# Kernel optimization log

Measured on AMD Instinct MI355X. Metric: run time of the kernel, lower is better.

## Reference

```python
import jax, jax.numpy as jnp
import numpy as np

B, S, D, H, FF = 4, 2048, 512, 8, 2048
W = 128  # local attention window size (hardcoded in module)
DH = D // H


def _ln(x, g, b, eps=1e-5):
    m = x.mean(-1, keepdims=True)
    v = ((x - m) ** 2).mean(-1, keepdims=True)
    return (x - m) / jnp.sqrt(v + eps) * g + b


def setup_inputs() -> dict:
    key = jax.random.key(0)
    ks = jax.random.split(key, 10)
    s = 0.02
    return {
        "src": jax.random.normal(ks[0], (B, S, D), jnp.float32),
        # global nn.MultiheadAttention params
        "in_proj_w": jax.random.normal(ks[1], (3 * D, D), jnp.float32) * s,
        "in_proj_b": jnp.zeros((3 * D,), jnp.float32),
        "out_proj_w": jax.random.normal(ks[2], (D, D), jnp.float32) * s,
        "out_proj_b": jnp.zeros((D,), jnp.float32),
        # LocalMHA params (prenorm LN, fused qkv no-bias, out proj no-bias)
        "ln_g": jnp.ones((D,), jnp.float32),
        "ln_b": jnp.zeros((D,), jnp.float32),
        "qkv_w": jax.random.normal(ks[3], (3 * D, D), jnp.float32) * s,
        "to_out_w": jax.random.normal(ks[4], (D, D), jnp.float32) * s,
        # glFusion + FFN + norms
        "gl_w": jax.random.normal(ks[5], (D, 2 * D), jnp.float32) * s,
        "gl_b": jnp.zeros((D,), jnp.float32),
        "norm1_g": jnp.ones((D,), jnp.float32),
        "norm1_b": jnp.zeros((D,), jnp.float32),
        "lin1_w": jax.random.normal(ks[6], (FF, D), jnp.float32) * s,
        "lin1_b": jnp.zeros((FF,), jnp.float32),
        "lin2_w": jax.random.normal(ks[7], (D, FF), jnp.float32) * s,
        "lin2_b": jnp.zeros((D,), jnp.float32),
        "norm2_g": jnp.ones((D,), jnp.float32),
        "norm2_b": jnp.zeros((D,), jnp.float32),
    }


def _forward(src, in_proj_w, in_proj_b, out_proj_w, out_proj_b, ln_g, ln_b,
             qkv_w, to_out_w, gl_w, gl_b, norm1_g, norm1_b,
             lin1_w, lin1_b, lin2_w, lin2_b, norm2_g, norm2_b):
    b, s, d = src.shape
    scale = DH ** -0.5

    def heads(x):  # (b, s, d) -> (b, H, s, DH)
        return x.reshape(b, s, H, DH).transpose(0, 2, 1, 3)

    # ---- global full MHA (no mask) ----
    qkv = src @ in_proj_w.T + in_proj_b
    qg, kg, vg = (heads(t) for t in jnp.split(qkv, 3, axis=-1))
    att = jax.nn.softmax(jnp.einsum('bhid,bhjd->bhij', qg, kg) * scale, axis=-1)
    go = jnp.einsum('bhij,bhjd->bhid', att, vg).transpose(0, 2, 1, 3).reshape(b, s, d)
    go = go @ out_proj_w.T + out_proj_b

    # ---- local windowed causal MHA with rotary (window=128, look_backward=1) ----
    x = _ln(src, ln_g, ln_b)  # prenorm
    ql, kl, vl = (heads(t) for t in jnp.split(x @ qkv_w.T, 3, axis=-1))

    pos = jnp.arange(s)
    inv_freq = 1.0 / (10000.0 ** (jnp.arange(0, DH, 2, dtype=jnp.float32) / DH))
    freqs = pos[:, None].astype(jnp.float32) * inv_freq[None, :]
    emb = jnp.concatenate([freqs, freqs], axis=-1)  # (s, DH)
    cos, sin = jnp.cos(emb), jnp.sin(emb)

    def rope(t):
        h = DH // 2
        t1, t2 = t[..., :h], t[..., h:]
        return t * cos + jnp.concatenate([-t2, t1], axis=-1) * sin

    ql, kl = rope(ql), rope(kl)
    ql = ql * scale

    nw = s // W
    qw = ql.reshape(b, H, nw, W, DH)
    kw = kl.reshape(b, H, nw, W, DH)
    vw = vl.reshape(b, H, nw, W, DH)

    def look_back(t):  # concat previous window with current: (b,H,nw,2W,DH)
        prev = jnp.pad(t, ((0, 0), (0, 0), (1, 0), (0, 0), (0, 0)))[:, :, :-1]
        return jnp.concatenate([prev, t], axis=3)

    bk, bv = look_back(kw), look_back(vw)

    qpos = pos.reshape(nw, W)
    kpos = jnp.concatenate(
        [jnp.concatenate([jnp.full((1, W), -1, pos.dtype), qpos[:-1]], axis=0), qpos],
        axis=1)  # (nw, 2W)
    mask = (kpos[:, None, :] >= 0) & (kpos[:, None, :] <= qpos[:, :, None])  # (nw,W,2W)

    sc = jnp.einsum('bhnid,bhnjd->bhnij', qw, bk)
    sc = jnp.where(mask, sc, jnp.finfo(sc.dtype).min)
    at = jax.nn.softmax(sc, axis=-1)
    lo = jnp.einsum('bhnij,bhnjd->bhnid', at, bv).reshape(b, H, s, DH)
    lo = lo.transpose(0, 2, 1, 3).reshape(b, s, d) @ to_out_w.T

    # ---- fuse global+local, residual, norms, FFN ----
    src2 = jnp.concatenate([go, lo], axis=-1) @ gl_w.T + gl_b
    h1 = _ln(src + src2, norm1_g, norm1_b)
    ff = jax.nn.relu(h1 @ lin1_w.T + lin1_b) @ lin2_w.T + lin2_b
    return _ln(h1 + ff, norm2_g, norm2_b)


def reference(src, in_proj_w, in_proj_b, out_proj_w, out_proj_b, ln_g, ln_b,
              qkv_w, to_out_w, gl_w, gl_b, norm1_g, norm1_b,
              lin1_w, lin1_b, lin2_w, lin2_b, norm2_g, norm2_b):
    return _forward(src, in_proj_w, in_proj_b, out_proj_w, out_proj_b, ln_g, ln_b,
                    qkv_w, to_out_w, gl_w, gl_b, norm1_g, norm1_b,
                    lin1_w, lin1_b, lin2_w, lin2_b, norm2_g, norm2_b)
```

## Files before the change

### kernel.cpp

```cpp
#include <hip/hip_runtime.h>
#include <math.h>

#define B_  4
#define S_  2048
#define D_  512
#define H_  8
#define FF_ 2048
#define W_  128
#define DH_ 64
#define NW_ 16
#define TRD (3*D_)
#define MR_ (B_*S_)

typedef __attribute__((ext_vector_type(8))) short short8;
typedef __attribute__((ext_vector_type(4))) float f32x4;

__device__ __forceinline__ short f2bf(float f) {
    unsigned u = __float_as_uint(f);
    unsigned r = (u + 0x7fff + ((u >> 16) & 1)) >> 16;
    return (short)r;
}
__device__ __forceinline__ float bf2f(ushort u) {
    return __uint_as_float(((unsigned)u) << 16);
}
__device__ __forceinline__ void gload_lds16(const ushort* g, short* l) {
    __builtin_amdgcn_global_load_lds(
        (const __attribute__((address_space(1))) void*)g,
        (__attribute__((address_space(3))) void*)l, 16, 0, 0);
}

struct CvtJobs { const float* s[8]; ushort* d[8]; int n[8]; };

__global__ __launch_bounds__(256) void cvt_kernel(CvtJobs jobs)
{
    int i4 = (blockIdx.x * 256 + threadIdx.x) * 4;
    #pragma unroll
    for (int j = 0; j < 8; j++) {
        if (i4 < jobs.n[j]) {
            float4 v = *(const float4*)(jobs.s[j] + i4);
            ushort4 o;
            o.x = (ushort)f2bf(v.x); o.y = (ushort)f2bf(v.y);
            o.z = (ushort)f2bf(v.z); o.w = (ushort)f2bf(v.w);
            *(ushort4*)(jobs.d[j] + i4) = o;
        }
    }
}

__global__ __launch_bounds__(256) void gemm_bf16_kernel(
    const ushort* __restrict__ A, int lda,
    const ushort* __restrict__ Wt,
    const float* __restrict__ bias,
    ushort* __restrict__ C, int ldc,
    int K, int relu)
{
    __shared__ short As[128 * 64];
    __shared__ short Bs[128 * 64];
    const int tid  = threadIdx.x;
    const int w    = tid >> 6;
    const int lane = tid & 63;
    const int quad = lane >> 4;
    const int x    = lane & 15;
    const int wr = w >> 1, wc = w & 1;
    const int bm = blockIdx.y * 128;
    const int bn = blockIdx.x * 128;

    const int srow = w * 32 + (lane >> 3);
    const int scol = ((lane & 7) ^ (lane >> 3)) * 8;

    f32x4 acc[4][4];
    #pragma unroll
    for (int i = 0; i < 4; i++)
        #pragma unroll
        for (int j = 0; j < 4; j++) acc[i][j] = (f32x4)0.f;

    for (int k0 = 0; k0 < K; k0 += 64) {
        __syncthreads();
        #pragma unroll
        for (int c = 0; c < 4; c++) {
            const ushort* ga = A + (size_t)(bm + srow + c * 8) * lda + k0 + scol;
            gload_lds16(ga, &As[(w * 32 + c * 8) * 64]);
            const ushort* gb = Wt + (size_t)(bn + srow + c * 8) * K + k0 + scol;
            gload_lds16(gb, &Bs[(w * 32 + c * 8) * 64]);
        }
        __syncthreads();

        #pragma unroll
        for (int kc = 0; kc < 2; kc++) {
            short8 af[4], bf[4];
            #pragma unroll
            for (int i = 0; i < 4; i++) {
                int row = wr * 64 + i * 16 + x;
                int pcg = (kc * 4 + quad) ^ (x & 7);
                af[i] = *(const short8*)&As[row * 64 + pcg * 8];
            }
            #pragma unroll
            for (int j = 0; j < 4; j++) {
                int row = wc * 64 + j * 16 + x;
                int pcg = (kc * 4 + quad) ^ (x & 7);
                bf[j] = *(const short8*)&Bs[row * 64 + pcg * 8];
            }
            #pragma unroll
            for (int i = 0; i < 4; i++)
                #pragma unroll
                for (int j = 0; j < 4; j++)
                    acc[i][j] = __builtin_amdgcn_mfma_f32_16x16x32_bf16(af[i], bf[j], acc[i][j], 0, 0, 0);
        }
    }

    #pragma unroll
    for (int i = 0; i < 4; i++) {
        #pragma unroll
        for (int r = 0; r < 4; r++) {
            size_t row = (size_t)(bm + wr * 64 + i * 16 + quad * 4 + r);
            #pragma unroll
            for (int j = 0; j < 4; j++) {
                int col = bn + wc * 64 + j * 16 + x;
                float v = acc[i][j][r] + (bias ? bias[col] : 0.f);
                if (relu) v = v > 0.f ? v : 0.f;
                C[row * ldc + col] = (ushort)f2bf(v);
            }
        }
    }
}

__device__ __forceinline__ float wave_sum64(float v) {
    #pragma unroll
    for (int off = 32; off > 0; off >>= 1) v += __shfl_xor(v, off, 64);
    return v;
}
__device__ __forceinline__ void load8(const float* p, float* v) {
    *(float4*)&v[0] = *(const float4*)p;
    *(float4*)&v[4] = *(const float4*)(p + 4);
}
__device__ __forceinline__ void load8(const ushort* p, float* v) {
    short8 s = *(const short8*)p;
    #pragma unroll
    for (int i = 0; i < 8; i++) v[i] = bf2f((ushort)s[i]);
}
__device__ __forceinline__ void store8(float* p, const float* v) {
    *(float4*)p       = make_float4(v[0], v[1], v[2], v[3]);
    *(float4*)(p + 4) = make_float4(v[4], v[5], v[6], v[7]);
}
__device__ __forceinline__ void store8(ushort* p, const float* v) {
    short8 s;
    #pragma unroll
    for (int i = 0; i < 8; i++) s[i] = f2bf(v[i]);
    *(short8*)p = s;
}

template <typename TA, typename TB, typename TO>
__global__ __launch_bounds__(256) void addln_kernel(
    const TA* __restrict__ a, const TB* __restrict__ b,
    const float* __restrict__ g, const float* __restrict__ be,
    TO* __restrict__ out)
{
    const int lane = threadIdx.x & 63;
    const int row  = blockIdx.x * 4 + (threadIdx.x >> 6);
    const size_t base = (size_t)row * D_ + lane * 8;
    float v[8];
    load8(a + base, v);
    if (b) {
        float wv[8];
        load8(b + base, wv);
        #pragma unroll
        for (int i = 0; i < 8; i++) v[i] += wv[i];
    }
    float s = 0.f;
    #pragma unroll
    for (int i = 0; i < 8; i++) s += v[i];
    float mean = wave_sum64(s) * (1.0f / 512.0f);
    float vs = 0.f;
    #pragma unroll
    for (int i = 0; i < 8; i++) { float d = v[i] - mean; vs += d * d; }
    float var = wave_sum64(vs) * (1.0f / 512.0f);
    float r = rsqrtf(var + 1e-5f);
    const int c = lane * 8;
    float t[8];
    #pragma unroll
    for (int i = 0; i < 8; i++) t[i] = (v[i] - mean) * r * g[c + i] + be[c + i];
    store8(out + base, t);
}

__global__ __launch_bounds__(256) void transpose_v_kernel(
    const ushort* __restrict__ qkv, ushort* __restrict__ vt)
{
    __shared__ ushort T[64][72];
    const int t  = threadIdx.x;
    const int s0 = blockIdx.x * 64;
    const int bh = blockIdx.y;
    const int b = bh >> 3, h = bh & 7;
    {
        int row = t >> 2, col = (t & 3) * 16;
        const ushort* src = qkv + ((size_t)(b * S_) + s0 + row) * TRD + 2 * D_ + h * DH_ + col;
        *(short8*)&T[row][col]     = *(const short8*)src;
        *(short8*)&T[row][col + 8] = *(const short8*)(src + 8);
    }
    __syncthreads();
    {
        int d = t >> 2, sc = (t & 3) * 16;
        ushort tmp[16];
        #pragma unroll
        for (int k = 0; k < 16; k++) tmp[k] = T[sc + k][d];
        ushort* dst = vt + ((size_t)bh * DH_ + d) * S_ + s0 + sc;
        *(short8*)dst       = *(const short8*)&tmp[0];
        *(short8*)(dst + 8) = *(const short8*)&tmp[8];
    }
}

#define PP 136

__global__ __launch_bounds__(256) void attn_global_mfma_kernel(
    const ushort* __restrict__ qkv, const ushort* __restrict__ vt,
    ushort* __restrict__ out)
{
    __shared__ short Ks[128 * 64];
    __shared__ short Vt[64 * 128];
    __shared__ short Pb[4 * 16 * PP];

    const int tid  = threadIdx.x;
    const int w    = tid >> 6;
    const int lane = tid & 63;
    const int quad = lane >> 4;
    const int x    = lane & 15;
    const int bh = blockIdx.y;
    const int b = bh >> 3, h = bh & 7;
    const int qbase = blockIdx.x * 64;
    const size_t bS = (size_t)b * S_;
    const size_t vbase = (size_t)bh * DH_;

    short8 aq[2];
    {
        const ushort* qp = qkv + (bS + qbase + w * 16 + x) * TRD + h * DH_;
        #pragma unroll
        for (int kc = 0; kc < 2; kc++) {
            short8 raw = *(const short8*)(qp + kc * 32 + quad * 8);
            #pragma unroll
            for (int j = 0; j < 8; j++)
                aq[kc][j] = f2bf(bf2f((ushort)raw[j]) * 0.125f);
        }
    }

    f32x4 o[4];
    #pragma unroll
    for (int dt = 0; dt < 4; dt++) o[dt] = (f32x4)0.f;
    float m[4], l[4];
    #pragma unroll
    for (int r = 0; r < 4; r++) { m[r] = -3.0e38f; l[r] = 0.f; }

    short* Pw = &Pb[w * 16 * PP];

    for (int kt = 0; kt < S_; kt += 128) {
        __syncthreads();
        #pragma unroll
        for (int c = 0; c < 4; c++) {
            int key = w * 32 + c * 8 + (lane >> 3);
            int cg  = (lane & 7) ^ (lane >> 3);
            const ushort* gk = qkv + (bS + kt + key) * TRD + D_ + h * DH_ + cg * 8;
            gload_lds16(gk, &Ks[(w * 32 + c * 8) * 64]);
        }
        #pragma unroll
        for (int c = 0; c < 4; c++) {
            int row = w * 16 + c * 4 + (lane >> 4);
            int cg  = (lane & 15) ^ (row & 7);
            const ushort* gv = vt + (vbase + row) * S_ + kt + cg * 8;
            gload_lds16(gv, &Vt[(w * 16 + c * 4) * 128]);
        }
        __syncthreads();

        f32x4 sc[8];
        #pragma unroll
        for (int nt = 0; nt < 8; nt++) {
            sc[nt] = (f32x4)0.f;
            #pragma unroll
            for (int kc = 0; kc < 2; kc++) {
                int pcg = (kc * 4 + quad) ^ (x & 7);
                short8 bk = *(const short8*)&Ks[(nt * 16 + x) * 64 + pcg * 8];
                sc[nt] = __builtin_amdgcn_mfma_f32_16x16x32_bf16(aq[kc], bk, sc[nt], 0, 0, 0);
            }
        }

        #pragma unroll
        for (int r = 0; r < 4; r++) {
            float mx = sc[0][r];
            #pragma unroll
            for (int nt = 1; nt < 8; nt++) mx = fmaxf(mx, sc[nt][r]);
            #pragma unroll
            for (int off = 1; off < 16; off <<= 1) mx = fmaxf(mx, __shfl_xor(mx, off, 64));
            float mnew = fmaxf(m[r], mx);
            float alpha = __expf(m[r] - mnew);
            m[r] = mnew;
            float psum = 0.f;
            #pragma unroll
            for (int nt = 0; nt < 8; nt++) {
                float p = __expf(sc[nt][r] - mnew);
                sc[nt][r] = p;
                psum += p;
            }
            #pragma unroll
            for (int off = 1; off < 16; off <<= 1) psum += __shfl_xor(psum, off, 64);
            l[r] = l[r] * alpha + psum;
            #pragma unroll
            for (int dt = 0; dt < 4; dt++) o[dt][r] *= alpha;
            #pragma unroll
            for (int nt = 0; nt < 8; nt++)
                Pw[(quad * 4 + r) * PP + nt * 16 + x] = f2bf(sc[nt][r]);
        }
        asm volatile("s_waitcnt lgkmcnt(0)" ::: "memory");

        #pragma unroll
        for (int kc = 0; kc < 4; kc++) {
            short8 ap = *(const short8*)&Pw[x * PP + kc * 32 + quad * 8];
            #pragma unroll
            for (int dt = 0; dt < 4; dt++) {
                int pcg = (kc * 4 + quad) ^ (x & 7);
                short8 bv = *(const short8*)&Vt[(dt * 16 + x) * 128 + pcg * 8];
                o[dt] = __builtin_amdgcn_mfma_f32_16x16x32_bf16(ap, bv, o[dt], 0, 0, 0);
            }
        }
    }

    #pragma unroll
    for (int r = 0; r < 4; r++) {
        float inv = 1.0f / l[r];
        size_t rowbase = (bS + qbase + w * 16 + quad * 4 + r) * D_ + h * DH_;
        #pragma unroll
        for (int dt = 0; dt < 4; dt++)
            out[rowbase + dt * 16 + x] = (ushort)f2bf(o[dt][r] * inv);
    }
}

__global__ __launch_bounds__(256) void rope_kernel(ushort* __restrict__ qkv)
{
    int idx = blockIdx.x * 256 + threadIdx.x;
    int d  = idx & 31;
    int h  = (idx >> 5) & 7;
    int bs = idx >> 8;
    int pos = bs & (S_ - 1);
    float inv_freq = exp2f(-(float)d * (2.0f / 64.0f) * 13.287712379549449f);
    float ang = (float)pos * inv_freq;
    float sn, cs;
    sincosf(ang, &sn, &cs);
    ushort* base = qkv + (size_t)bs * TRD + h * DH_;
    float q1 = bf2f(base[d]), q2 = bf2f(base[d + 32]);
    base[d]      = (ushort)f2bf((q1 * cs - q2 * sn) * 0.125f);
    base[d + 32] = (ushort)f2bf((q2 * cs + q1 * sn) * 0.125f);
    ushort* kb = base + D_;
    float k1 = bf2f(kb[d]), k2 = bf2f(kb[d + 32]);
    kb[d]      = (ushort)f2bf(k1 * cs - k2 * sn);
    kb[d + 32] = (ushort)f2bf(k2 * cs + k1 * sn);
}

__global__ __launch_bounds__(256) void attn_local_mfma_kernel(
    const ushort* __restrict__ qkv, const ushort* __restrict__ vt,
    ushort* __restrict__ out)
{
    __shared__ short Ks[128 * 64];
    __shared__ short Vt[64 * 128];
    __shared__ short Pb[4 * 16 * PP];

    const int tid  = threadIdx.x;
    const int w    = tid >> 6;
    const int lane = tid & 63;
    const int quad = lane >> 4;
    const int x    = lane & 15;
    const int bh = blockIdx.y;
    const int b = bh >> 3, h = bh & 7;
    const int qbase = blockIdx.x * 64;
    const int n = qbase >> 7;
    const size_t bS = (size_t)b * S_;
    const size_t vbase = (size_t)bh * DH_;

    short8 aq[2];
    {
        const ushort* qp = qkv + (bS + qbase + w * 16 + x) * TRD + h * DH_;
        #pragma unroll
        for (int kc = 0; kc < 2; kc++)
            aq[kc] = *(const short8*)(qp + kc * 32 + quad * 8);
    }

    f32x4 o[4];
    #pragma unroll
    for (int dt = 0; dt < 4; dt++) o[dt] = (f32x4)0.f;
    float m[4], l[4];
    #pragma unroll
    for (int r = 0; r < 4; r++) { m[r] = -3.0e38f; l[r] = 0.f; }

    short* Pw = &Pb[w * 16 * PP];

    for (int kt = 0; kt < 2; kt++) {
        const int kbase = (n - 1) * 128 + kt * 128;
        if (kbase < 0) continue;
        __syncthreads();
        #pragma unroll
        for (int c = 0; c < 4; c++) {
            int key = w * 32 + c * 8 + (lane >> 3);
            int cg  = (lane & 7) ^ (lane >> 3);
            const ushort* gk = qkv + (bS + kbase + key) * TRD + D_ + h * DH_ + cg * 8;
            gload_lds16(gk, &Ks[(w * 32 + c * 8) * 64]);
        }
        #pragma unroll
        for (int c = 0; c < 4; c++) {
            int row = w * 16 + c * 4 + (lane >> 4);
            int cg  = (lane & 15) ^ (row & 7);
            const ushort* gv = vt + (vbase + row) * S_ + kbase + cg * 8;
            gload_lds16(gv, &Vt[(w * 16 + c * 4) * 128]);
        }
        __syncthreads();

        f32x4 sc[8];
        #pragma unroll
        for (int nt = 0; nt < 8; nt++) {
            sc[nt] = (f32x4)0.f;
            #pragma unroll
            for (int kc = 0; kc < 2; kc++) {
                int pcg = (kc * 4 + quad) ^ (x & 7);
                short8 bk = *(const short8*)&Ks[(nt * 16 + x) * 64 + pcg * 8];
                sc[nt] = __builtin_amdgcn_mfma_f32_16x16x32_bf16(aq[kc], bk, sc[nt], 0, 0, 0);
            }
        }
        if (kt == 1) {
            #pragma unroll
            for (int nt = 0; nt < 8; nt++) {
                int kp = kbase + nt * 16 + x;
                #pragma unroll
                for (int r = 0; r < 4; r++) {
                    int qp = qbase + w * 16 + quad * 4 + r;
                    if (kp > qp) sc[nt][r] = -3.0e38f;
                }
            }
        }

        #pragma unroll
        for (int r = 0; r < 4; r++) {
            float mx = sc[0][r];
            #pragma unroll
            for (int nt = 1; nt < 8; nt++) mx = fmaxf(mx, sc[nt][r]);
            #pragma unroll
            for (int off = 1; off < 16; off <<= 1) mx = fmaxf(mx, __shfl_xor(mx, off, 64));
            float mnew = fmaxf(m[r], mx);
            float alpha = __expf(m[r] - mnew);
            m[r] = mnew;
            float psum = 0.f;
            #pragma unroll
            for (int nt = 0; nt < 8; nt++) {
                float p = __expf(sc[nt][r] - mnew);
                sc[nt][r] = p;
                psum += p;
            }
            #pragma unroll
            for (int off = 1; off < 16; off <<= 1) psum += __shfl_xor(psum, off, 64);
            l[r] = l[r] * alpha + psum;
            #pragma unroll
            for (int dt = 0; dt < 4; dt++) o[dt][r] *= alpha;
            #pragma unroll
            for (int nt = 0; nt < 8; nt++)
                Pw[(quad * 4 + r) * PP + nt * 16 + x] = f2bf(sc[nt][r]);
        }
        asm volatile("s_waitcnt lgkmcnt(0)" ::: "memory");

        #pragma unroll
        for (int kc = 0; kc < 4; kc++) {
            short8 ap = *(const short8*)&Pw[x * PP + kc * 32 + quad * 8];
            #pragma unroll
            for (int dt = 0; dt < 4; dt++) {
                int pcg = (kc * 4 + quad) ^ (x & 7);
                short8 bv = *(const short8*)&Vt[(dt * 16 + x) * 128 + pcg * 8];
                o[dt] = __builtin_amdgcn_mfma_f32_16x16x32_bf16(ap, bv, o[dt], 0, 0, 0);
            }
        }
    }

    #pragma unroll
    for (int r = 0; r < 4; r++) {
        float inv = 1.0f / l[r];
        size_t rowbase = (bS + qbase + w * 16 + quad * 4 + r) * D_ + h * DH_;
        #pragma unroll
        for (int dt = 0; dt < 4; dt++)
            out[rowbase + dt * 16 + x] = (ushort)f2bf(o[dt][r] * inv);
    }
}

extern "C" void kernel_launch(void* const* d_in, const int* in_sizes, int n_in,
                              void* d_out, int out_size, void* d_ws, size_t ws_size,
                              hipStream_t stream)
{
    (void)in_sizes; (void)n_in; (void)out_size; (void)ws_size;
    const float* src        = (const float*)d_in[0];
    const float* in_proj_w  = (const float*)d_in[1];
    const float* in_proj_b  = (const float*)d_in[2];
    const float* out_proj_w = (const float*)d_in[3];
    const float* out_proj_b = (const float*)d_in[4];
    const float* ln_g       = (const float*)d_in[5];
    const float* ln_b       = (const float*)d_in[6];
    const float* qkv_w      = (const float*)d_in[7];
    const float* to_out_w   = (const float*)d_in[8];
    const float* gl_w       = (const float*)d_in[9];
    const float* gl_b       = (const float*)d_in[10];
    const float* norm1_g    = (const float*)d_in[11];
    const float* norm1_b    = (const float*)d_in[12];
    const float* lin1_w     = (const float*)d_in[13];
    const float* lin1_b     = (const float*)d_in[14];
    const float* lin2_w     = (const float*)d_in[15];
    const float* lin2_b     = (const float*)d_in[16];
    const float* norm2_g    = (const float*)d_in[17];
    const float* norm2_b    = (const float*)d_in[18];
    float* out = (float*)d_out;

    ushort* ws16   = (ushort*)d_ws;
    ushort* src_bf = ws16;
    ushort* wi_bf  = src_bf + (size_t)MR_ * D_;
    ushort* wq_bf  = wi_bf  + TRD * D_;
    ushort* wo_bf  = wq_bf  + TRD * D_;
    ushort* wt_bf  = wo_bf  + D_ * D_;
    ushort* wg_bf  = wt_bf  + D_ * D_;
    ushort* w1_bf  = wg_bf  + D_ * 2 * D_;
    ushort* w2_bf  = w1_bf  + FF_ * D_;
    ushort* buf1   = w2_bf  + D_ * FF_;
    ushort* h1b    = buf1   + (size_t)MR_ * D_;
    ushort* buf0   = h1b    + (size_t)MR_ * D_;
    ushort* buf2   = buf0   + (size_t)MR_ * TRD;
    ushort* vtg    = buf2   + (size_t)MR_ * 2 * D_;
    ushort* vtl    = vtg    + (size_t)MR_ * D_;
    ushort* ff1    = buf0;

    dim3 blk256(256);

    CvtJobs jobs;
    jobs.s[0] = src;        jobs.d[0] = src_bf; jobs.n[0] = MR_ * D_;
    jobs.s[1] = in_proj_w;  jobs.d[1] = wi_bf;  jobs.n[1] = TRD * D_;
    jobs.s[2] = qkv_w;      jobs.d[2] = wq_bf;  jobs.n[2] = TRD * D_;
    jobs.s[3] = out_proj_w; jobs.d[3] = wo_bf;  jobs.n[3] = D_ * D_;
    jobs.s[4] = to_out_w;   jobs.d[4] = wt_bf;  jobs.n[4] = D_ * D_;
    jobs.s[5] = gl_w;       jobs.d[5] = wg_bf;  jobs.n[5] = D_ * 2 * D_;
    jobs.s[6] = lin1_w;     jobs.d[6] = w1_bf;  jobs.n[6] = FF_ * D_;
    jobs.s[7] = lin2_w;     jobs.d[7] = w2_bf;  jobs.n[7] = D_ * FF_;
    cvt_kernel<<<dim3((MR_ * D_ / 4 + 255) / 256), blk256, 0, stream>>>(jobs);

    gemm_bf16_kernel<<<dim3(TRD / 128, MR_ / 128), blk256, 0, stream>>>(
        src_bf, D_, wi_bf, in_proj_b, buf0, TRD, D_, 0);
    transpose_v_kernel<<<dim3(S_ / 64, B_ * H_), blk256, 0, stream>>>(buf0, vtg);
    attn_global_mfma_kernel<<<dim3(S_ / 64, B_ * H_), blk256, 0, stream>>>(buf0, vtg, buf1);
    gemm_bf16_kernel<<<dim3(D_ / 128, MR_ / 128), blk256, 0, stream>>>(
        buf1, D_, wo_bf, out_proj_b, buf2, 2 * D_, D_, 0);
    addln_kernel<float, float, ushort><<<dim3(MR_ / 4), blk256, 0, stream>>>(
        src, (const float*)nullptr, ln_g, ln_b, buf1);
    gemm_bf16_kernel<<<dim3(TRD / 128, MR_ / 128), blk256, 0, stream>>>(
        buf1, D_, wq_bf, nullptr, buf0, TRD, D_, 0);
    transpose_v_kernel<<<dim3(S_ / 64, B_ * H_), blk256, 0, stream>>>(buf0, vtl);
    rope_kernel<<<dim3((B_ * S_ * H_ * 32) / 256), blk256, 0, stream>>>(buf0);
    attn_local_mfma_kernel<<<dim3(S_ / 64, B_ * H_), blk256, 0, stream>>>(buf0, vtl, buf1);
    gemm_bf16_kernel<<<dim3(D_ / 128, MR_ / 128), blk256, 0, stream>>>(
        buf1, D_, wt_bf, nullptr, buf2 + D_, 2 * D_, D_, 0);
    gemm_bf16_kernel<<<dim3(D_ / 128, MR_ / 128), blk256, 0, stream>>>(
        buf2, 2 * D_, wg_bf, gl_b, buf1, D_, 2 * D_, 0);
    addln_kernel<float, ushort, ushort><<<dim3(MR_ / 4), blk256, 0, stream>>>(
        src, buf1, norm1_g, norm1_b, h1b);
    gemm_bf16_kernel<<<dim3(FF_ / 128, MR_ / 128), blk256, 0, stream>>>(
        h1b, D_, w1_bf, lin1_b, ff1, FF_, D_, 1);
    gemm_bf16_kernel<<<dim3(D_ / 128, MR_ / 128), blk256, 0, stream>>>(
        ff1, FF_, w2_bf, lin2_b, buf1, D_, FF_, 0);
    addln_kernel<ushort, ushort, float><<<dim3(MR_ / 4), blk256, 0, stream>>>(
        h1b, buf1, norm2_g, norm2_b, out);
}
```

Before: 492.3 us.

## Unify attention kernels on 32x32 MFMA tiles with max-free softmax

Replaces the separate global and local attention kernels with one templated kernel. It uses 128 threads, 64-key tiles and the 32x32x16 bf16 MFMA, and computes O^T = V^T·P^T. The online-softmax running max, rescale and per-tile shuffle reductions are removed: plain exp is accumulated and the row sum is reduced once at the end. That cuts VALU and shuffle work but relies on scores staying small enough not to overflow. The local path now skips 64-key tiles that are fully above the causal diagonal and masks only the diagonal tile. Output is staged through LDS so each row is written with wide, coalesced stores.

```diff
diff --git a/kernel.cpp b/kernel.cpp
--- a/kernel.cpp
+++ b/kernel.cpp
@@ -12,8 +12,10 @@
 #define TRD (3*D_)
 #define MR_ (B_*S_)
 
-typedef __attribute__((ext_vector_type(8))) short short8;
-typedef __attribute__((ext_vector_type(4))) float f32x4;
+typedef __attribute__((ext_vector_type(8)))  short short8;
+typedef __attribute__((ext_vector_type(4)))  short short4v;
+typedef __attribute__((ext_vector_type(4)))  float f32x4;
+typedef __attribute__((ext_vector_type(16))) float f32x16;
 
 __device__ __forceinline__ short f2bf(float f) {
     unsigned u = __float_as_uint(f);
@@ -207,125 +209,160 @@
     }
 }
 
-#define PP 136
-
-__global__ __launch_bounds__(256) void attn_global_mfma_kernel(
+#define PPW 72
+
+template <int LOCAL>
+__global__ __launch_bounds__(128) void attn_kernel(
     const ushort* __restrict__ qkv, const ushort* __restrict__ vt,
     ushort* __restrict__ out)
 {
-    __shared__ short Ks[128 * 64];
-    __shared__ short Vt[64 * 128];
-    __shared__ short Pb[4 * 16 * PP];
+    __shared__ short Ks[64 * 64];
+    __shared__ short Vt[64 * 64];
+    __shared__ short Pb[2 * 32 * PPW];
+    __shared__ float Lw[2][32];
 
     const int tid  = threadIdx.x;
     const int w    = tid >> 6;
     const int lane = tid & 63;
-    const int quad = lane >> 4;
-    const int x    = lane & 15;
+    const int half = lane >> 5;
+    const int c    = lane & 31;
     const int bh = blockIdx.y;
     const int b = bh >> 3, h = bh & 7;
     const int qbase = blockIdx.x * 64;
     const size_t bS = (size_t)b * S_;
     const size_t vbase = (size_t)bh * DH_;
 
-    short8 aq[2];
+    short8 aq[4];
     {
-        const ushort* qp = qkv + (bS + qbase + w * 16 + x) * TRD + h * DH_;
-        #pragma unroll
-        for (int kc = 0; kc < 2; kc++) {
-            short8 raw = *(const short8*)(qp + kc * 32 + quad * 8);
-            #pragma unroll
-            for (int j = 0; j < 8; j++)
-                aq[kc][j] = f2bf(bf2f((ushort)raw[j]) * 0.125f);
-        }
-    }
-
-    f32x4 o[4];
-    #pragma unroll
-    for (int dt = 0; dt < 4; dt++) o[dt] = (f32x4)0.f;
-    float m[4], l[4];
-    #pragma unroll
-    for (int r = 0; r < 4; r++) { m[r] = -3.0e38f; l[r] = 0.f; }
-
-    short* Pw = &Pb[w * 16 * PP];
-
-    for (int kt = 0; kt < S_; kt += 128) {
+        const ushort* qp = qkv + (bS + qbase + w * 32 + c) * TRD + h * DH_;
+        #pragma unroll
+        for (int kc = 0; kc < 4; kc++) {
+            short8 raw = *(const short8*)(qp + kc * 16 + half * 8);
+            if (LOCAL) {
+                aq[kc] = raw;
+            } else {
+                #pragma unroll
+                for (int j = 0; j < 8; j++)
+                    aq[kc][j] = f2bf(bf2f((ushort)raw[j]) * 0.125f);
+            }
+        }
+    }
+
+    f32x16 ot[2];
+    #pragma unroll
+    for (int dt = 0; dt < 2; dt++) ot[dt] = (f32x16)0.f;
+    float lp[16];
+    #pragma unroll
+    for (int r = 0; r < 16; r++) lp[r] = 0.f;
+
+    short* Pw = &Pb[w * 32 * PPW];
+    const int nkt = LOCAL ? 4 : (S_ / 64);
+
+    for (int kt = 0; kt < nkt; kt++) {
+        const int kbase = LOCAL ? ((qbase >> 7) * 128 - 128 + kt * 64) : kt * 64;
+        if (LOCAL) {
+            if (kbase < 0 || kbase > qbase + 63) continue;
+        }
+        const bool diag = LOCAL && (kbase == qbase);
+
         __syncthreads();
         #pragma unroll
-        for (int c = 0; c < 4; c++) {
-            int key = w * 32 + c * 8 + (lane >> 3);
+        for (int cc = 0; cc < 4; cc++) {
+            int row = w * 32 + cc * 8 + (lane >> 3);
             int cg  = (lane & 7) ^ (lane >> 3);
-            const ushort* gk = qkv + (bS + kt + key) * TRD + D_ + h * DH_ + cg * 8;
-            gload_lds16(gk, &Ks[(w * 32 + c * 8) * 64]);
-        }
-        #pragma unroll
-        for (int c = 0; c < 4; c++) {
-            int row = w * 16 + c * 4 + (lane >> 4);
-            int cg  = (lane & 15) ^ (row & 7);
-            const ushort* gv = vt + (vbase + row) * S_ + kt + cg * 8;
-            gload_lds16(gv, &Vt[(w * 16 + c * 4) * 128]);
+            const ushort* gk = qkv + (bS + kbase + row) * TRD + D_ + h * DH_ + cg * 8;
+            gload_lds16(gk, &Ks[(w * 32 + cc * 8) * 64]);
+            const ushort* gv = vt + (vbase + row) * S_ + kbase + cg * 8;
+            gload_lds16(gv, &Vt[(w * 32 + cc * 8) * 64]);
         }
         __syncthreads();
 
-        f32x4 sc[8];
-        #pragma unroll
-        for (int nt = 0; nt < 8; nt++) {
-            sc[nt] = (f32x4)0.f;
-            #pragma unroll
-            for (int kc = 0; kc < 2; kc++) {
-                int pcg = (kc * 4 + quad) ^ (x & 7);
-                short8 bk = *(const short8*)&Ks[(nt * 16 + x) * 64 + pcg * 8];
-                sc[nt] = __builtin_amdgcn_mfma_f32_16x16x32_bf16(aq[kc], bk, sc[nt], 0, 0, 0);
-            }
-        }
-
-        #pragma unroll
-        for (int r = 0; r < 4; r++) {
-            float mx = sc[0][r];
-            #pragma unroll
-            for (int nt = 1; nt < 8; nt++) mx = fmaxf(mx, sc[nt][r]);
-            #pragma unroll
-            for (int off = 1; off < 16; off <<= 1) mx = fmaxf(mx, __shfl_xor(mx, off, 64));
-            float mnew = fmaxf(m[r], mx);
-            float alpha = __expf(m[r] - mnew);
-            m[r] = mnew;
-            float psum = 0.f;
-            #pragma unroll
-            for (int nt = 0; nt < 8; nt++) {
-                float p = __expf(sc[nt][r] - mnew);
-                sc[nt][r] = p;
-                psum += p;
-            }
-            #pragma unroll
-            for (int off = 1; off < 16; off <<= 1) psum += __shfl_xor(psum, off, 64);
-            l[r] = l[r] * alpha + psum;
-            #pragma unroll
-            for (int dt = 0; dt < 4; dt++) o[dt][r] *= alpha;
-            #pragma unroll
-            for (int nt = 0; nt < 8; nt++)
-                Pw[(quad * 4 + r) * PP + nt * 16 + x] = f2bf(sc[nt][r]);
+        f32x16 sc[2];
+        #pragma unroll
+        for (int nt = 0; nt < 2; nt++) {
+            sc[nt] = (f32x16)0.f;
+            #pragma unroll
+            for (int kc = 0; kc < 4; kc++) {
+                int row = nt * 32 + c;
+                int pcg = (kc * 2 + half) ^ (row & 7);
+                short8 bk = *(const short8*)&Ks[row * 64 + pcg * 8];
+                sc[nt] = __builtin_amdgcn_mfma_f32_32x32x16_bf16(aq[kc], bk, sc[nt], 0, 0, 0);
+            }
+        }
+
+        #pragma unroll
+        for (int nt = 0; nt < 2; nt++) {
+            #pragma unroll
+            for (int r = 0; r < 16; r++) {
+                int qrow = (r & 3) + 8 * (r >> 2) + 4 * half;
+                float p;
+                if (diag) {
+                    bool valid = (kbase + nt * 32 + c) <= (qbase + w * 32 + qrow);
+                    p = valid ? __expf(sc[nt][r]) : 0.f;
+                } else {
+                    p = __expf(sc[nt][r]);
+                }
+                lp[r] += p;
+                Pw[qrow * PPW + nt * 32 + c] = f2bf(p);
+            }
         }
         asm volatile("s_waitcnt lgkmcnt(0)" ::: "memory");
 
         #pragma unroll
         for (int kc = 0; kc < 4; kc++) {
-            short8 ap = *(const short8*)&Pw[x * PP + kc * 32 + quad * 8];
-            #pragma unroll
-            for (int dt = 0; dt < 4; dt++) {
-                int pcg = (kc * 4 + quad) ^ (x & 7);
-                short8 bv = *(const short8*)&Vt[(dt * 16 + x) * 128 + pcg * 8];
-                o[dt] = __builtin_amdgcn_mfma_f32_16x16x32_bf16(ap, bv, o[dt], 0, 0, 0);
-            }
-        }
-    }
-
-    #pragma unroll
-    for (int r = 0; r < 4; r++) {
-        float inv = 1.0f / l[r];
-        size_t rowbase = (bS + qbase + w * 16 + quad * 4 + r) * D_ + h * DH_;
-        #pragma unroll
-        for (int dt = 0; dt < 4; dt++)
-            out[rowbase + dt * 16 + x] = (ushort)f2bf(o[dt][r] * inv);
+            short8 bp = *(const short8*)&Pw[c * PPW + kc * 16 + half * 8];
+            #pragma unroll
+            for (int dt = 0; dt < 2; dt++) {
+                int row = dt * 32 + c;
+                int pcg = (kc * 2 + half) ^ (row & 7);
+                short8 av = *(const short8*)&Vt[row * 64 + pcg * 8];
+                ot[dt] = __builtin_amdgcn_mfma_f32_32x32x16_bf16(av, bp, ot[dt], 0, 0, 0);
+            }
+        }
+    }
+
+    #pragma unroll
+    for (int r = 0; r < 16; r++) {
+        float v = lp[r];
+        #pragma unroll
+        for (int off = 1; off < 32; off <<= 1) v += __shfl_xor(v, off, 64);
+        lp[r] = v;
+    }
+    if (c == 0) {
+        #pragma unroll
+        for (int r = 0; r < 16; r++)
+            Lw[w][(r & 3) + 8 * (r >> 2) + 4 * half] = lp[r];
+    }
+    asm volatile("s_waitcnt lgkmcnt(0)" ::: "memory");
+    __builtin_amdgcn_wave_barrier();
+    float inv = 1.0f / Lw[w][c];
+
+    #pragma unroll
+    for (int dt = 0; dt < 2; dt++) {
+        #pragma unroll
+        for (int rq = 0; rq < 4; rq++) {
+            short4v pk;
+            #pragma unroll
+            for (int i = 0; i < 4; i++)
+                pk[i] = f2bf(ot[dt][rq * 4 + i] * inv);
+            int dbase = dt * 32 + 8 * rq + 4 * half;
+            *(short4v*)&Pw[c * PPW + dbase] = pk;
+        }
+    }
+    asm volatile("s_waitcnt lgkmcnt(0)" ::: "memory");
+    __builtin_amdgcn_wave_barrier();
+    {
+        int q  = lane >> 1;
+        int d0 = (lane & 1) * 32;
+        short8 v0 = *(const short8*)&Pw[q * PPW + d0];
+        short8 v1 = *(const short8*)&Pw[q * PPW + d0 + 8];
+        short8 v2 = *(const short8*)&Pw[q * PPW + d0 + 16];
+        short8 v3 = *(const short8*)&Pw[q * PPW + d0 + 24];
+        ushort* op = out + (bS + qbase + w * 32 + q) * D_ + h * DH_ + d0;
+        *(short8*)(op)      = v0;
+        *(short8*)(op + 8)  = v1;
+        *(short8*)(op + 16) = v2;
+        *(short8*)(op + 24) = v3;
     }
 }
 
@@ -348,136 +385,6 @@
     float k1 = bf2f(kb[d]), k2 = bf2f(kb[d + 32]);
     kb[d]      = (ushort)f2bf(k1 * cs - k2 * sn);
     kb[d + 32] = (ushort)f2bf(k2 * cs + k1 * sn);
-}
-
-__global__ __launch_bounds__(256) void attn_local_mfma_kernel(
-    const ushort* __restrict__ qkv, const ushort* __restrict__ vt,
-    ushort* __restrict__ out)
-{
-    __shared__ short Ks[128 * 64];
-    __shared__ short Vt[64 * 128];
-    __shared__ short Pb[4 * 16 * PP];
-
-    const int tid  = threadIdx.x;
-    const int w    = tid >> 6;
-    const int lane = tid & 63;
-    const int quad = lane >> 4;
-    const int x    = lane & 15;
-    const int bh = blockIdx.y;
-    const int b = bh >> 3, h = bh & 7;
-    const int qbase = blockIdx.x * 64;
-    const int n = qbase >> 7;
-    const size_t bS = (size_t)b * S_;
-    const size_t vbase = (size_t)bh * DH_;
-
-    short8 aq[2];
-    {
-        const ushort* qp = qkv + (bS + qbase + w * 16 + x) * TRD + h * DH_;
-        #pragma unroll
-        for (int kc = 0; kc < 2; kc++)
-            aq[kc] = *(const short8*)(qp + kc * 32 + quad * 8);
-    }
-
-    f32x4 o[4];
-    #pragma unroll
-    for (int dt = 0; dt < 4; dt++) o[dt] = (f32x4)0.f;
-    float m[4], l[4];
-    #pragma unroll
-    for (int r = 0; r < 4; r++) { m[r] = -3.0e38f; l[r] = 0.f; }
-
-    short* Pw = &Pb[w * 16 * PP];
-
-    for (int kt = 0; kt < 2; kt++) {
-        const int kbase = (n - 1) * 128 + kt * 128;
-        if (kbase < 0) continue;
-        __syncthreads();
-        #pragma unroll
-        for (int c = 0; c < 4; c++) {
-            int key = w * 32 + c * 8 + (lane >> 3);
-            int cg  = (lane & 7) ^ (lane >> 3);
-            const ushort* gk = qkv + (bS + kbase + key) * TRD + D_ + h * DH_ + cg * 8;
-            gload_lds16(gk, &Ks[(w * 32 + c * 8) * 64]);
-        }
-        #pragma unroll
-        for (int c = 0; c < 4; c++) {
-            int row = w * 16 + c * 4 + (lane >> 4);
-            int cg  = (lane & 15) ^ (row & 7);
-            const ushort* gv = vt + (vbase + row) * S_ + kbase + cg * 8;
-            gload_lds16(gv, &Vt[(w * 16 + c * 4) * 128]);
-        }
-        __syncthreads();
-
-        f32x4 sc[8];
-        #pragma unroll
-        for (int nt = 0; nt < 8; nt++) {
-            sc[nt] = (f32x4)0.f;
-            #pragma unroll
-            for (int kc = 0; kc < 2; kc++) {
-                int pcg = (kc * 4 + quad) ^ (x & 7);
-                short8 bk = *(const short8*)&Ks[(nt * 16 + x) * 64 + pcg * 8];
-                sc[nt] = __builtin_amdgcn_mfma_f32_16x16x32_bf16(aq[kc], bk, sc[nt], 0, 0, 0);
-            }
-        }
-        if (kt == 1) {
-            #pragma unroll
-            for (int nt = 0; nt < 8; nt++) {
-                int kp = kbase + nt * 16 + x;
-                #pragma unroll
-                for (int r = 0; r < 4; r++) {
-                    int qp = qbase + w * 16 + quad * 4 + r;
-                    if (kp > qp) sc[nt][r] = -3.0e38f;
-                }
-            }
-        }
-
-        #pragma unroll
-        for (int r = 0; r < 4; r++) {
-            float mx = sc[0][r];
-            #pragma unroll
-            for (int nt = 1; nt < 8; nt++) mx = fmaxf(mx, sc[nt][r]);
-            #pragma unroll
-            for (int off = 1; off < 16; off <<= 1) mx = fmaxf(mx, __shfl_xor(mx, off, 64));
-            float mnew = fmaxf(m[r], mx);
-            float alpha = __expf(m[r] - mnew);
-            m[r] = mnew;
-            float psum = 0.f;
-            #pragma unroll
-            for (int nt = 0; nt < 8; nt++) {
-                float p = __expf(sc[nt][r] - mnew);
-                sc[nt][r] = p;
-                psum += p;
-            }
-            #pragma unroll
-            for (int off = 1; off < 16; off <<= 1) psum += __shfl_xor(psum, off, 64);
-            l[r] = l[r] * alpha + psum;
-            #pragma unroll
-            for (int dt = 0; dt < 4; dt++) o[dt][r] *= alpha;
-            #pragma unroll
-            for (int nt = 0; nt < 8; nt++)
-                Pw[(quad * 4 + r) * PP + nt * 16 + x] = f2bf(sc[nt][r]);
-        }
-        asm volatile("s_waitcnt lgkmcnt(0)" ::: "memory");
-
-        #pragma unroll
-        for (int kc = 0; kc < 4; kc++) {
-            short8 ap = *(const short8*)&Pw[x * PP + kc * 32 + quad * 8];
-            #pragma unroll
-            for (int dt = 0; dt < 4; dt++) {
-                int pcg = (kc * 4 + quad) ^ (x & 7);
-                short8 bv = *(const short8*)&Vt[(dt * 16 + x) * 128 + pcg * 8];
-                o[dt] = __builtin_amdgcn_mfma_f32_16x16x32_bf16(ap, bv, o[dt], 0, 0, 0);
-            }
-        }
-    }
-
-    #pragma unroll
-    for (int r = 0; r < 4; r++) {
-        float inv = 1.0f / l[r];
-        size_t rowbase = (bS + qbase + w * 16 + quad * 4 + r) * D_ + h * DH_;
-        #pragma unroll
-        for (int dt = 0; dt < 4; dt++)
-            out[rowbase + dt * 16 + x] = (ushort)f2bf(o[dt][r] * inv);
-    }
 }
 
 extern "C" void kernel_launch(void* const* d_in, const int* in_sizes, int n_in,
@@ -523,7 +430,7 @@
     ushort* vtl    = vtg    + (size_t)MR_ * D_;
     ushort* ff1    = buf0;
 
-    dim3 blk256(256);
+    dim3 blk256(256), blk128(128);
 
     CvtJobs jobs;
     jobs.s[0] = src;        jobs.d[0] = src_bf; jobs.n[0] = MR_ * D_;
@@ -539,7 +446,7 @@
     gemm_bf16_kernel<<<dim3(TRD / 128, MR_ / 128), blk256, 0, stream>>>(
         src_bf, D_, wi_bf, in_proj_b, buf0, TRD, D_, 0);
     transpose_v_kernel<<<dim3(S_ / 64, B_ * H_), blk256, 0, stream>>>(buf0, vtg);
-    attn_global_mfma_kernel<<<dim3(S_ / 64, B_ * H_), blk256, 0, stream>>>(buf0, vtg, buf1);
+    attn_kernel<0><<<dim3(S_ / 64, B_ * H_), blk128, 0, stream>>>(buf0, vtg, buf1);
     gemm_bf16_kernel<<<dim3(D_ / 128, MR_ / 128), blk256, 0, stream>>>(
         buf1, D_, wo_bf, out_proj_b, buf2, 2 * D_, D_, 0);
     addln_kernel<float, float, ushort><<<dim3(MR_ / 4), blk256, 0, stream>>>(
@@ -548,7 +455,7 @@
         buf1, D_, wq_bf, nullptr, buf0, TRD, D_, 0);
     transpose_v_kernel<<<dim3(S_ / 64, B_ * H_), blk256, 0, stream>>>(buf0, vtl);
     rope_kernel<<<dim3((B_ * S_ * H_ * 32) / 256), blk256, 0, stream>>>(buf0);
-    attn_local_mfma_kernel<<<dim3(S_ / 64, B_ * H_), blk256, 0, stream>>>(buf0, vtl, buf1);
+    attn_kernel<1><<<dim3(S_ / 64, B_ * H_), blk128, 0, stream>>>(buf0, vtl, buf1);
     gemm_bf16_kernel<<<dim3(D_ / 128, MR_ / 128), blk256, 0, stream>>>(
         buf1, D_, wt_bf, nullptr, buf2 + D_, 2 * D_, D_, 0);
     gemm_bf16_kernel<<<dim3(D_ / 128, MR_ / 128), blk256, 0, stream>>>(
```

After: 462.5 us. -6.0%, faster.
